# Kernel tuning notes

Measured on AMD Instinct MI355X. Metric: run time of the kernel, lower is better.

The kernel has to match this reference:

```python
import jax, jax.numpy as jnp
import numpy as np

B, S, IN, OUT, H, M = 16, 512, 512, 512, 8, 4
HF = OUT // H  # head_feats = 64


def setup_inputs() -> dict:
    key = jax.random.key(0)
    ks = jax.random.split(key, 12)
    std = 0.02
    queries = jax.random.normal(ks[0], (B, S, IN), jnp.float32)
    keys = jax.random.normal(ks[1], (B, S, IN), jnp.float32)
    timespans = jax.random.uniform(ks[2], (B, S), jnp.float32)
    # causal mask tiled over heads*batch, matching [H*B, S, S] score shape
    attention_masks = jnp.broadcast_to(jnp.tril(jnp.ones((S, S), jnp.float32)), (H * B, S, S))
    event_marks = jax.random.uniform(ks[3], (H * B, 1, S, M), jnp.float32)
    Wq = std * jax.random.normal(ks[4], (IN, OUT), jnp.float32)
    Wk = std * jax.random.normal(ks[5], (IN, OUT), jnp.float32)
    Wv = std * jax.random.normal(ks[6], (IN, OUT), jnp.float32)
    Wt = std * jax.random.normal(ks[7], (IN, OUT), jnp.float32)
    Wi = std * jax.random.normal(ks[8], (HF + 1, M * HF), jnp.float32)  # fc_i weight
    bi = jnp.zeros((M * HF,), jnp.float32)                               # fc_i bias
    weight_i = std * jax.random.normal(ks[9], (M, HF), jnp.float32)
    scale_i = jnp.zeros((M,), jnp.float32)
    return {"queries": queries, "keys": keys, "timespans": timespans,
            "attention_masks": attention_masks, "event_marks": event_marks,
            "Wq": Wq, "Wk": Wk, "Wv": Wv, "Wt": Wt, "Wi": Wi, "bi": bi,
            "weight_i": weight_i, "scale_i": scale_i}


def reference(queries, keys, timespans, attention_masks, event_marks,
              Wq, Wk, Wv, Wt, Wi, bi, weight_i, scale_i):
    # torch's cat(chunk(X, H, dim=2), dim=0) == [B,S,H,HF] -> [H,B,S,HF] -> flat h*B+b
    def split_heads(X):
        return X.reshape(B, S, H, HF).transpose(2, 0, 1, 3)  # [H,B,S,HF]

    Q = split_heads(queries @ Wq)
    K = split_heads(keys @ Wk)
    V = split_heads(keys @ Wv)
    T = split_heads(keys @ Wt)

    scores = jnp.einsum('hbqf,hbkf->hbqk', Q, K) / jnp.sqrt(jnp.float32(OUT))
    mask = attention_masks.reshape(H, B, S, S)
    scores = jnp.where(mask == 0.0, jnp.float32(-2 ** 32 + 1), scores)
    attn = jax.nn.softmax(scores, axis=-1)  # [H,B,Sq,Sk]

    E = jnp.einsum('hbqk,hbkf->hbqf', attn, T)  # events fed to intensity net

    # --- Hawkes intensities ---
    ts = jnp.broadcast_to(timespans[None, :, :, None], (H, B, S, 1))
    mu = jax.nn.sigmoid(jnp.concatenate([E, ts], axis=-1) @ Wi + bi)  # [H,B,S,M*HF]
    mu = mu.reshape(H, B, S, M, HF)  # chunk over marks along feature dim
    scale = jnp.exp(scale_i)  # [M]
    lam = jnp.einsum('hbsmf,mf->hbsm', mu, weight_i) / scale
    lam = scale * jnp.log1p(jnp.exp(lam))  # scaled softplus, [H,B,S,M]

    # mark_inty[h,b,q,k] = sum_m lam[h,b,q,m] * event_marks[h,b,k,m]
    em = event_marks.reshape(H, B, S, M)
    mark_inty = jnp.einsum('hbqm,hbkm->hbqk', lam, em)

    out = jnp.einsum('hbqk,hbkf->hbqf', attn * mark_inty, V)
    out = out.transpose(1, 2, 0, 3).reshape(B, S, OUT) + queries[..., :OUT]
    all_mark_inty = lam.reshape(H * B, S, M)
    return out, all_mark_inty
```

## Files before the change

### kernel.cpp

```cpp
#include <hip/hip_runtime.h>
#include <math.h>

typedef __attribute__((ext_vector_type(8))) short short8;
typedef __attribute__((ext_vector_type(4))) float f32x4;

static __device__ __forceinline__ unsigned short f2bf(float f) {
  unsigned int u = __float_as_uint(f);
  u += 0x7FFFu + ((u >> 16) & 1u);
  return (unsigned short)(u >> 16);
}

static __device__ __forceinline__ void cp16(void* lds, const void* g) {
  __builtin_amdgcn_global_load_lds((const __attribute__((address_space(1))) void*)g,
                                   (__attribute__((address_space(3))) void*)lds,
                                   16, 0, 0);
}

__global__ __launch_bounds__(256) void convert_k(
    const float* __restrict__ Wq, const float* __restrict__ Wk,
    const float* __restrict__ Wv, const float* __restrict__ Wt,
    const float* __restrict__ Wi,
    unsigned short* __restrict__ Wb, unsigned short* __restrict__ WiF)
{
  __shared__ unsigned short tr[64 * 68];
  const int blk = blockIdx.x, tid = threadIdx.x;
  if (blk < 256) {
    int which = blk >> 6, tile = blk & 63;
    int r0 = (tile >> 3) << 6, c0 = (tile & 7) << 6;
    const float* W = (which == 0) ? Wq : (which == 1) ? Wk : (which == 2) ? Wv : Wt;
    const int rr = tid >> 4, cc = (tid & 15) << 2;
#pragma unroll
    for (int u = 0; u < 4; ++u) {
      int r = rr + u * 16;
      float4 v = *(const float4*)(W + (size_t)(r0 + r) * 512 + c0 + cc);
      tr[(cc + 0) * 68 + r] = f2bf(v.x);
      tr[(cc + 1) * 68 + r] = f2bf(v.y);
      tr[(cc + 2) * 68 + r] = f2bf(v.z);
      tr[(cc + 3) * 68 + r] = f2bf(v.w);
    }
    __syncthreads();
    unsigned short* dst = Wb + which * 262144;
#pragma unroll
    for (int u = 0; u < 4; ++u) {
      int c = rr + u * 16;
      ushort4 o = *(const ushort4*)&tr[c * 68 + cc];
      *(ushort4*)(dst + (size_t)(c0 + c) * 512 + r0 + cc) = o;
    }
  } else {
    int e = (blk - 256) * 256 + tid;
    int j = e & 7, ll = (e >> 3) & 63, r = e >> 9;
    int kk = r % 3, nt = r / 3;
    int col = nt * 16 + (ll & 15);
    int k = kk * 32 + (ll >> 4) * 8 + j;
    float val = (k < 64) ? Wi[k * 256 + col] : ((k == 64) ? Wi[16384 + col] : 0.0f);
    WiF[e] = f2bf(val);
  }
}

__global__ __launch_bounds__(256) void proj_mfma(
    const float* __restrict__ qin, const float* __restrict__ kin,
    const unsigned short* __restrict__ Wb,
    unsigned short* __restrict__ Qg, unsigned short* __restrict__ Kg,
    unsigned short* __restrict__ Vt, unsigned short* __restrict__ Tt)
{
  const int which = blockIdx.z;
  const float* A = (which == 0) ? qin : kin;
  const unsigned short* W = Wb + which * 262144;
  const int row0 = blockIdx.x * 128;
  const int col0 = blockIdx.y * 128;
  const int tid = threadIdx.x;
  const int wv = tid >> 6, l = tid & 63;
  const int quad = l >> 4, lc = l & 15;
  const int wm = wv >> 1, wn = wv & 1;

  __shared__ unsigned short Asm[2][128 * 32];
  __shared__ unsigned short Bsm[2][128 * 32];

  const int e2 = tid + 256;
  const int br0 = tid >> 2, bg0 = (tid & 3) ^ (br0 & 3);
  const int br1 = e2 >> 2,  bg1 = (e2 & 3) ^ (br1 & 3);
  f32x4 acc[4][4] = {};

  cp16(&Bsm[0][tid * 8], W + (size_t)(col0 + br0) * 512 + bg0 * 8);
  cp16(&Bsm[0][e2 * 8], W + (size_t)(col0 + br1) * 512 + bg1 * 8);
#pragma unroll
  for (int u = 0; u < 4; ++u) {
    int i = tid + u * 256, r = i >> 3, c4 = i & 7;
    float4 v = *(const float4*)(A + (size_t)(row0 + r) * 512 + c4 * 4);
    ushort4 o;
    o.x = f2bf(v.x); o.y = f2bf(v.y); o.z = f2bf(v.z); o.w = f2bf(v.w);
    *(ushort4*)&Asm[0][r * 32 + (((c4 >> 1) ^ (r & 3)) << 3) + ((c4 & 1) << 2)] = o;
  }
  __syncthreads();

  const int xk = lc & 3;
  for (int ks = 0; ks < 16; ++ks) {
    const int cur = ks & 1, nxt = cur ^ 1;
    float4 av[4];
    if (ks < 15) {
      const int k1 = (ks + 1) << 5;
      cp16(&Bsm[nxt][tid * 8], W + (size_t)(col0 + br0) * 512 + k1 + bg0 * 8);
      cp16(&Bsm[nxt][e2 * 8], W + (size_t)(col0 + br1) * 512 + k1 + bg1 * 8);
#pragma unroll
      for (int u = 0; u < 4; ++u) {
        int i = tid + u * 256, r = i >> 3, c4 = i & 7;
        av[u] = *(const float4*)(A + (size_t)(row0 + r) * 512 + k1 + c4 * 4);
      }
    }
    short8 a[4], b[4];
#pragma unroll
    for (int mi = 0; mi < 4; ++mi)
      a[mi] = *(const short8*)&Asm[cur][(wm * 64 + mi * 16 + lc) * 32 + ((quad ^ xk) << 3)];
#pragma unroll
    for (int nj = 0; nj < 4; ++nj)
      b[nj] = *(const short8*)&Bsm[cur][(wn * 64 + nj * 16 + lc) * 32 + ((quad ^ xk) << 3)];
#pragma unroll
    for (int mi = 0; mi < 4; ++mi)
#pragma unroll
      for (int nj = 0; nj < 4; ++nj)
        acc[mi][nj] = __builtin_amdgcn_mfma_f32_16x16x32_bf16(a[mi], b[nj], acc[mi][nj], 0, 0, 0);
    if (ks < 15) {
#pragma unroll
      for (int u = 0; u < 4; ++u) {
        int i = tid + u * 256, r = i >> 3, c4 = i & 7;
        ushort4 o;
        o.x = f2bf(av[u].x); o.y = f2bf(av[u].y); o.z = f2bf(av[u].z); o.w = f2bf(av[u].w);
        *(ushort4*)&Asm[nxt][r * 32 + (((c4 >> 1) ^ (r & 3)) << 3) + ((c4 & 1) << 2)] = o;
      }
    }
    __syncthreads();
  }

  const int h = (col0 >> 6) + wn;
  const int bidx = row0 >> 9;
  const int hb = h * 16 + bidx;
  if (which < 2) {
    unsigned short* C = (which == 0) ? Qg : Kg;
    const float os = (which == 0) ? 0.044194173824159216f : 1.0f;
#pragma unroll
    for (int mi = 0; mi < 4; ++mi) {
      int sbase = (row0 & 511) + wm * 64 + mi * 16 + quad * 4;
#pragma unroll
      for (int nj = 0; nj < 4; ++nj) {
        size_t base = (size_t)hb * 32768 + (size_t)sbase * 64 + nj * 16 + lc;
#pragma unroll
        for (int reg = 0; reg < 4; ++reg)
          C[base + (size_t)reg * 64] = f2bf(acc[mi][nj][reg] * os);
      }
    }
  } else {
    unsigned short* C = (which == 2) ? Vt : Tt;
    unsigned short* scr = wn ? Bsm[0] : Asm[0];
    const int sb = (row0 & 511) + wm * 64;
    __syncthreads();
#pragma unroll
    for (int round = 0; round < 2; ++round) {
      if (wm == round) {
#pragma unroll
        for (int mi = 0; mi < 4; ++mi)
#pragma unroll
          for (int nj = 0; nj < 4; ++nj)
#pragma unroll
            for (int reg = 0; reg < 4; ++reg) {
              int f = nj * 16 + lc, s = mi * 16 + quad * 4 + reg;
              int g = (s >> 3) ^ (f & 7);
              scr[f * 64 + g * 8 + (s & 7)] = f2bf(acc[mi][nj][reg]);
            }
#pragma unroll
        for (int it = 0; it < 8; ++it) {
          int fl = it * 8 + (l >> 3);
          int gg = (l & 7) ^ (fl & 7);
          short8 v = *(const short8*)&scr[fl * 64 + gg * 8];
          *(short8*)(C + (size_t)hb * 32768 + (size_t)fl * 512 + sb + (l & 7) * 8) = v;
        }
      }
      __syncthreads();
    }
  }
}

__global__ __launch_bounds__(256, 2) void attn_fused(
    const unsigned short* __restrict__ Qg, const unsigned short* __restrict__ Kg,
    const unsigned short* __restrict__ Vtg, const unsigned short* __restrict__ Ttg,
    const unsigned short* __restrict__ WiF,
    const float* __restrict__ bi, const float* __restrict__ wim,
    const float* __restrict__ sci, const float* __restrict__ tsp,
    const float* __restrict__ em, const float* __restrict__ queries,
    float* __restrict__ out, float* __restrict__ lamout)
{
  const int hb = blockIdx.x;
  const int y = blockIdx.y;
  const int qb = (y == 0) ? 3 : (y == 1) ? 2 : (y == 2) ? 0 : 1;
  const int q0 = qb << 7;
  const int kts = 2 * qb + 2;
  const int tid = threadIdx.x, wv = tid >> 6, l = tid & 63;
  const int quad = l >> 4, lc = l & 15;
  const int xg = lc & 7;

  __shared__ unsigned short Qs[8192];
  __shared__ unsigned short Ks[2][4096];
  __shared__ unsigned short TVs[2][4096];
  __shared__ unsigned short Wl[4][3072];
  __shared__ float emS[2][256];

  const int e1 = tid + 256;
  const int sr0 = tid >> 3, sg0 = (tid & 7) ^ (sr0 & 7);
  const int sr1 = e1 >> 3,  sg1 = (e1 & 7) ^ (sr1 & 7);
  const int sqk0 = sr0 * 64 + sg0 * 8,  sqk1 = sr1 * 64 + sg1 * 8;
  const int stv0 = sr0 * 512 + sg0 * 8, stv1 = sr1 * 512 + sg1 * 8;

  const unsigned short* KgB = Kg + (size_t)hb * 32768;
  const unsigned short* TgB = Ttg + (size_t)hb * 32768;
  const unsigned short* VgB = Vtg + (size_t)hb * 32768;

  const unsigned short* Qbase = Qg + (size_t)hb * 32768 + q0 * 64;
#pragma unroll
  for (int u = 0; u < 4; ++u) {
    int e = tid + u * 256;
    int r = e >> 3, g = (e & 7) ^ (r & 7);
    cp16(&Qs[e * 8], Qbase + r * 64 + g * 8);
  }
  cp16(&Ks[0][tid * 8], KgB + sqk0);
  cp16(&Ks[0][e1 * 8], KgB + sqk1);
  cp16(&TVs[0][tid * 8], TgB + stv0);
  cp16(&TVs[0][e1 * 8], TgB + stv1);
  __syncthreads();

  short8 aq[2][2];
#pragma unroll
  for (int rt = 0; rt < 2; ++rt)
#pragma unroll
    for (int kk = 0; kk < 2; ++kk)
      aq[rt][kk] = *(const short8*)&Qs[(wv * 32 + rt * 16 + lc) * 64 + ((kk * 4 + quad) ^ xg) * 8];

  f32x4 Eacc[2][4] = {};
  float lsum[2][4] = {};

  for (int kt = 0; kt < kts; ++kt) {
    const int cur = kt & 1, nxt = cur ^ 1;
    const int k0 = kt << 6;
    if (kt + 1 < kts) {
      const int k1 = (kt + 1) << 6;
      cp16(&Ks[nxt][tid * 8], KgB + k1 * 64 + sqk0);
      cp16(&Ks[nxt][e1 * 8], KgB + k1 * 64 + sqk1);
      cp16(&TVs[nxt][tid * 8], TgB + k1 + stv0);
      cp16(&TVs[nxt][e1 * 8], TgB + k1 + stv1);
    }
    f32x4 sc[2][4] = {};
#pragma unroll
    for (int kk = 0; kk < 2; ++kk)
#pragma unroll
      for (int nj = 0; nj < 4; ++nj) {
        short8 b = *(const short8*)&Ks[cur][(nj * 16 + lc) * 64 + ((kk * 4 + quad) ^ xg) * 8];
        sc[0][nj] = __builtin_amdgcn_mfma_f32_16x16x32_bf16(aq[0][kk], b, sc[0][nj], 0, 0, 0);
        sc[1][nj] = __builtin_amdgcn_mfma_f32_16x16x32_bf16(aq[1][kk], b, sc[1][nj], 0, 0, 0);
      }
#pragma unroll
    for (int rt = 0; rt < 2; ++rt) {
      const int gq = q0 + wv * 32 + rt * 16 + quad * 4;
#pragma unroll
      for (int nj = 0; nj < 4; ++nj) {
        int col = nj * 16 + lc;
#pragma unroll
        for (int reg = 0; reg < 4; ++reg) {
          float pv = __expf(sc[rt][nj][reg]);
          if (k0 + col > gq + reg) pv = 0.0f;
          lsum[rt][reg] += pv;
          int row = rt * 16 + quad * 4 + reg;
          int gp = (nj * 2 + (lc >> 3)) ^ (row & 7);
          Wl[wv][row * 96 + gp * 8 + (lc & 7)] = f2bf(pv);
        }
      }
    }
#pragma unroll
    for (int rt = 0; rt < 2; ++rt)
#pragma unroll
      for (int kk = 0; kk < 2; ++kk) {
        short8 a = *(const short8*)&Wl[wv][(rt * 16 + lc) * 96 + ((kk * 4 + quad) ^ xg) * 8];
#pragma unroll
        for (int fj = 0; fj < 4; ++fj) {
          short8 b = *(const short8*)&TVs[cur][(fj * 16 + lc) * 64 + ((kk * 4 + quad) ^ xg) * 8];
          Eacc[rt][fj] = __builtin_amdgcn_mfma_f32_16x16x32_bf16(a, b, Eacc[rt][fj], 0, 0, 0);
        }
      }
    __syncthreads();
  }

  float inv[2][4];
#pragma unroll
  for (int rt = 0; rt < 2; ++rt)
#pragma unroll
    for (int reg = 0; reg < 4; ++reg) {
      float s = lsum[rt][reg];
#pragma unroll
      for (int off = 1; off < 16; off <<= 1) s += __shfl_xor(s, off);
      inv[rt][reg] = 1.0f / s;
    }

#pragma unroll
  for (int rt = 0; rt < 2; ++rt)
#pragma unroll
    for (int reg = 0; reg < 4; ++reg) {
      int row = rt * 16 + quad * 4 + reg;
      int gq = q0 + wv * 32 + rt * 16 + quad * 4;
      unsigned short* rp = &Wl[wv][row * 96];
#pragma unroll
      for (int fj = 0; fj < 4; ++fj) {
        int gp = (fj * 2 + (lc >> 3)) ^ (row & 7);
        rp[gp * 8 + (lc & 7)] = f2bf(Eacc[rt][fj][reg] * inv[rt][reg]);
      }
      float tsv = (lc == 0) ? tsp[(hb & 15) * 512 + gq + reg] : 0.0f;
      int gt = 8 + ((lc >> 3) ^ (row & 3));
      rp[gt * 8 + (lc & 7)] = f2bf(tsv);
      int gz = 8 + ((2 + (lc >> 3)) ^ (row & 3));
      rp[gz * 8 + (lc & 7)] = 0;
    }

  float lam4[2][4][4];
#pragma unroll
  for (int rt = 0; rt < 2; ++rt) {
    short8 ia[3];
    ia[0] = *(const short8*)&Wl[wv][(rt * 16 + lc) * 96 + ((0 + quad) ^ xg) * 8];
    ia[1] = *(const short8*)&Wl[wv][(rt * 16 + lc) * 96 + ((4 + quad) ^ xg) * 8];
    ia[2] = *(const short8*)&Wl[wv][(rt * 16 + lc) * 96 + (8 + (quad ^ (lc & 3))) * 8];
    float lac[4][4] = {};
#pragma unroll
    for (int nt = 0; nt < 16; ++nt) {
      f32x4 iacc = {};
#pragma unroll
      for (int kk = 0; kk < 3; ++kk) {
        short8 b = *(const short8*)(WiF + ((nt * 3 + kk) * 64 + l) * 8);
        iacc = __builtin_amdgcn_mfma_f32_16x16x32_bf16(ia[kk], b, iacc, 0, 0, 0);
      }
      float bvv = bi[nt * 16 + lc];
      float wmv = wim[nt * 16 + lc];
#pragma unroll
      for (int reg = 0; reg < 4; ++reg) {
        float mu = 1.0f / (1.0f + __expf(-(iacc[reg] + bvv)));
        lac[reg][nt >> 2] += mu * wmv;
      }
    }
#pragma unroll
    for (int m = 0; m < 4; ++m) {
      float scv = __expf(sci[m]);
#pragma unroll
      for (int reg = 0; reg < 4; ++reg) {
        float s = lac[reg][m];
#pragma unroll
        for (int off = 1; off < 16; off <<= 1) s += __shfl_xor(s, off);
        float z = s / scv;
        float sp = (z > 20.0f) ? z : log1pf(__expf(z));
        lam4[rt][reg][m] = scv * sp;
      }
    }
    if (lc < 4) {
      int gq = q0 + wv * 32 + rt * 16 + quad * 4;
#pragma unroll
      for (int reg = 0; reg < 4; ++reg) {
        float v = (lc == 0) ? lam4[rt][reg][0] : (lc == 1) ? lam4[rt][reg][1]
                : (lc == 2) ? lam4[rt][reg][2] : lam4[rt][reg][3];
        lamout[((size_t)hb * 512 + gq + reg) * 4 + lc] = v;
      }
    }
#pragma unroll
    for (int reg = 0; reg < 4; ++reg)
#pragma unroll
      for (int m = 0; m < 4; ++m)
        lam4[rt][reg][m] *= inv[rt][reg];
  }

  cp16(&Ks[0][tid * 8], KgB + sqk0);
  cp16(&Ks[0][e1 * 8], KgB + sqk1);
  cp16(&TVs[0][tid * 8], VgB + stv0);
  cp16(&TVs[0][e1 * 8], VgB + stv1);
  emS[0][tid] = em[(size_t)hb * 2048 + tid];
  __syncthreads();

  f32x4 Oacc[2][4] = {};
  for (int kt = 0; kt < kts; ++kt) {
    const int cur = kt & 1, nxt = cur ^ 1;
    const int k0 = kt << 6;
    if (kt + 1 < kts) {
      const int k1 = (kt + 1) << 6;
      cp16(&Ks[nxt][tid * 8], KgB + k1 * 64 + sqk0);
      cp16(&Ks[nxt][e1 * 8], KgB + k1 * 64 + sqk1);
      cp16(&TVs[nxt][tid * 8], VgB + k1 + stv0);
      cp16(&TVs[nxt][e1 * 8], VgB + k1 + stv1);
      emS[nxt][tid] = em[(size_t)hb * 2048 + k1 * 4 + tid];
    }
    f32x4 sc[2][4] = {};
#pragma unroll
    for (int kk = 0; kk < 2; ++kk)
#pragma unroll
      for (int nj = 0; nj < 4; ++nj) {
        short8 b = *(const short8*)&Ks[cur][(nj * 16 + lc) * 64 + ((kk * 4 + quad) ^ xg) * 8];
        sc[0][nj] = __builtin_amdgcn_mfma_f32_16x16x32_bf16(aq[0][kk], b, sc[0][nj], 0, 0, 0);
        sc[1][nj] = __builtin_amdgcn_mfma_f32_16x16x32_bf16(aq[1][kk], b, sc[1][nj], 0, 0, 0);
      }
#pragma unroll
    for (int rt = 0; rt < 2; ++rt) {
      const int gq = q0 + wv * 32 + rt * 16 + quad * 4;
#pragma unroll
      for (int nj = 0; nj < 4; ++nj) {
        int col = nj * 16 + lc;
        float4 emv = *(const float4*)&emS[cur][col * 4];
#pragma unroll
        for (int reg = 0; reg < 4; ++reg) {
          float pv = __expf(sc[rt][nj][reg]);
          if (k0 + col > gq + reg) pv = 0.0f;
          float mk = lam4[rt][reg][0] * emv.x + lam4[rt][reg][1] * emv.y +
                     lam4[rt][reg][2] * emv.z + lam4[rt][reg][3] * emv.w;
          int row = rt * 16 + quad * 4 + reg;
          int gp = (nj * 2 + (lc >> 3)) ^ (row & 7);
          Wl[wv][row * 96 + gp * 8 + (lc & 7)] = f2bf(pv * mk);
        }
      }
    }
#pragma unroll
    for (int rt = 0; rt < 2; ++rt)
#pragma unroll
      for (int kk = 0; kk < 2; ++kk) {
        short8 a = *(const short8*)&Wl[wv][(rt * 16 + lc) * 96 + ((kk * 4 + quad) ^ xg) * 8];
#pragma unroll
        for (int fj = 0; fj < 4; ++fj) {
          short8 b = *(const short8*)&TVs[cur][(fj * 16 + lc) * 64 + ((kk * 4 + quad) ^ xg) * 8];
          Oacc[rt][fj] = __builtin_amdgcn_mfma_f32_16x16x32_bf16(a, b, Oacc[rt][fj], 0, 0, 0);
        }
      }
    __syncthreads();
  }

  const int h = hb >> 4, bidx = hb & 15;
#pragma unroll
  for (int rt = 0; rt < 2; ++rt) {
    const int gq = q0 + wv * 32 + rt * 16 + quad * 4;
#pragma unroll
    for (int reg = 0; reg < 4; ++reg) {
      size_t o = (size_t)bidx * 262144 + (size_t)(gq + reg) * 512 + h * 64 + lc;
#pragma unroll
      for (int fj = 0; fj < 4; ++fj)
        out[o + fj * 16] = Oacc[rt][fj][reg] + queries[o + fj * 16];
    }
  }
}

extern "C" void kernel_launch(void* const* d_in, const int* in_sizes, int n_in,
                              void* d_out, int out_size, void* d_ws, size_t ws_size,
                              hipStream_t stream)
{
  (void)in_sizes; (void)n_in; (void)out_size; (void)ws_size;
  const float* queries = (const float*)d_in[0];
  const float* keys    = (const float*)d_in[1];
  const float* tsp     = (const float*)d_in[2];
  const float* em      = (const float*)d_in[4];
  const float* Wq      = (const float*)d_in[5];
  const float* Wk      = (const float*)d_in[6];
  const float* Wv      = (const float*)d_in[7];
  const float* Wt      = (const float*)d_in[8];
  const float* Wi      = (const float*)d_in[9];
  const float* bi      = (const float*)d_in[10];
  const float* wim     = (const float*)d_in[11];
  const float* sci     = (const float*)d_in[12];
  float* out = (float*)d_out;

  char* w = (char*)d_ws;
  unsigned short* Qg  = (unsigned short*)(w + 0);
  unsigned short* Kg  = (unsigned short*)(w + 8388608);
  unsigned short* Vt  = (unsigned short*)(w + 16777216);
  unsigned short* Tt  = (unsigned short*)(w + 25165824);
  unsigned short* Wb  = (unsigned short*)(w + 33554432);
  unsigned short* WiF = (unsigned short*)(w + 35651584);

  convert_k<<<352, 256, 0, stream>>>(Wq, Wk, Wv, Wt, Wi, Wb, WiF);
  proj_mfma<<<dim3(64, 4, 4), 256, 0, stream>>>(queries, keys, Wb, Qg, Kg, Vt, Tt);
  attn_fused<<<dim3(128, 4), 256, 0, stream>>>(Qg, Kg, Vt, Tt, WiF, bi, wim, sci,
                                               tsp, em, queries, out,
                                               out + 4194304);
}
```

Before: 303.4 us.

## Skip fully masked causal tiles per wave, fold log2e into weights, add setprio

```diff
diff --git a/kernel.cpp b/kernel.cpp
--- a/kernel.cpp
+++ b/kernel.cpp
@@ -3,11 +3,24 @@
 
 typedef __attribute__((ext_vector_type(8))) short short8;
 typedef __attribute__((ext_vector_type(4))) float f32x4;
+
+#define L2E 1.4426950408889634f
 
 static __device__ __forceinline__ unsigned short f2bf(float f) {
   unsigned int u = __float_as_uint(f);
   u += 0x7FFFu + ((u >> 16) & 1u);
   return (unsigned short)(u >> 16);
+}
+
+static __device__ __forceinline__ float fast_exp2(float x) {
+#if __has_builtin(__builtin_amdgcn_exp2f)
+  return __builtin_amdgcn_exp2f(x);
+#else
+  return exp2f(x);
+#endif
+}
+static __device__ __forceinline__ float fast_rcp(float x) {
+  return __builtin_amdgcn_rcpf(x);
 }
 
 static __device__ __forceinline__ void cp16(void* lds, const void* g) {
@@ -53,7 +66,7 @@
     int col = nt * 16 + (ll & 15);
     int k = kk * 32 + (ll >> 4) * 8 + j;
     float val = (k < 64) ? Wi[k * 256 + col] : ((k == 64) ? Wi[16384 + col] : 0.0f);
-    WiF[e] = f2bf(val);
+    WiF[e] = f2bf(val * L2E);
   }
 }
 
@@ -114,11 +127,13 @@
 #pragma unroll
     for (int nj = 0; nj < 4; ++nj)
       b[nj] = *(const short8*)&Bsm[cur][(wn * 64 + nj * 16 + lc) * 32 + ((quad ^ xk) << 3)];
+    __builtin_amdgcn_s_setprio(1);
 #pragma unroll
     for (int mi = 0; mi < 4; ++mi)
 #pragma unroll
       for (int nj = 0; nj < 4; ++nj)
         acc[mi][nj] = __builtin_amdgcn_mfma_f32_16x16x32_bf16(a[mi], b[nj], acc[mi][nj], 0, 0, 0);
+    __builtin_amdgcn_s_setprio(0);
     if (ks < 15) {
 #pragma unroll
       for (int u = 0; u < 4; ++u) {
@@ -136,7 +151,7 @@
   const int hb = h * 16 + bidx;
   if (which < 2) {
     unsigned short* C = (which == 0) ? Qg : Kg;
-    const float os = (which == 0) ? 0.044194173824159216f : 1.0f;
+    const float os = (which == 0) ? 0.044194173824159216f * L2E : 1.0f;
 #pragma unroll
     for (int mi = 0; mi < 4; ++mi) {
       int sbase = (row0 & 511) + wm * 64 + mi * 16 + quad * 4;
@@ -196,8 +211,8 @@
   const int tid = threadIdx.x, wv = tid >> 6, l = tid & 63;
   const int quad = l >> 4, lc = l & 15;
   const int xg = lc & 7;
-
-  __shared__ unsigned short Qs[8192];
+  const int wrow0 = q0 + wv * 32;
+
   __shared__ unsigned short Ks[2][4096];
   __shared__ unsigned short TVs[2][4096];
   __shared__ unsigned short Wl[4][3072];
@@ -213,25 +228,21 @@
   const unsigned short* TgB = Ttg + (size_t)hb * 32768;
   const unsigned short* VgB = Vtg + (size_t)hb * 32768;
 
-  const unsigned short* Qbase = Qg + (size_t)hb * 32768 + q0 * 64;
-#pragma unroll
-  for (int u = 0; u < 4; ++u) {
-    int e = tid + u * 256;
-    int r = e >> 3, g = (e & 7) ^ (r & 7);
-    cp16(&Qs[e * 8], Qbase + r * 64 + g * 8);
-  }
   cp16(&Ks[0][tid * 8], KgB + sqk0);
   cp16(&Ks[0][e1 * 8], KgB + sqk1);
   cp16(&TVs[0][tid * 8], TgB + stv0);
   cp16(&TVs[0][e1 * 8], TgB + stv1);
+
+  short8 aq[2][2];
+  {
+    const unsigned short* Qp = Qg + (size_t)hb * 32768;
+#pragma unroll
+    for (int rt = 0; rt < 2; ++rt)
+#pragma unroll
+      for (int kk = 0; kk < 2; ++kk)
+        aq[rt][kk] = *(const short8*)(Qp + (size_t)(wrow0 + rt * 16 + lc) * 64 + (kk * 4 + quad) * 8);
+  }
   __syncthreads();
-
-  short8 aq[2][2];
-#pragma unroll
-  for (int rt = 0; rt < 2; ++rt)
-#pragma unroll
-    for (int kk = 0; kk < 2; ++kk)
-      aq[rt][kk] = *(const short8*)&Qs[(wv * 32 + rt * 16 + lc) * 64 + ((kk * 4 + quad) ^ xg) * 8];
 
   f32x4 Eacc[2][4] = {};
   float lsum[2][4] = {};
@@ -246,43 +257,62 @@
       cp16(&TVs[nxt][tid * 8], TgB + k1 + stv0);
       cp16(&TVs[nxt][e1 * 8], TgB + k1 + stv1);
     }
-    f32x4 sc[2][4] = {};
-#pragma unroll
-    for (int kk = 0; kk < 2; ++kk)
-#pragma unroll
-      for (int nj = 0; nj < 4; ++nj) {
-        short8 b = *(const short8*)&Ks[cur][(nj * 16 + lc) * 64 + ((kk * 4 + quad) ^ xg) * 8];
-        sc[0][nj] = __builtin_amdgcn_mfma_f32_16x16x32_bf16(aq[0][kk], b, sc[0][nj], 0, 0, 0);
-        sc[1][nj] = __builtin_amdgcn_mfma_f32_16x16x32_bf16(aq[1][kk], b, sc[1][nj], 0, 0, 0);
-      }
-#pragma unroll
-    for (int rt = 0; rt < 2; ++rt) {
-      const int gq = q0 + wv * 32 + rt * 16 + quad * 4;
-#pragma unroll
-      for (int nj = 0; nj < 4; ++nj) {
-        int col = nj * 16 + lc;
-#pragma unroll
-        for (int reg = 0; reg < 4; ++reg) {
-          float pv = __expf(sc[rt][nj][reg]);
-          if (k0 + col > gq + reg) pv = 0.0f;
-          lsum[rt][reg] += pv;
-          int row = rt * 16 + quad * 4 + reg;
-          int gp = (nj * 2 + (lc >> 3)) ^ (row & 7);
-          Wl[wv][row * 96 + gp * 8 + (lc & 7)] = f2bf(pv);
-        }
-      }
-    }
-#pragma unroll
-    for (int rt = 0; rt < 2; ++rt)
-#pragma unroll
-      for (int kk = 0; kk < 2; ++kk) {
-        short8 a = *(const short8*)&Wl[wv][(rt * 16 + lc) * 96 + ((kk * 4 + quad) ^ xg) * 8];
-#pragma unroll
-        for (int fj = 0; fj < 4; ++fj) {
-          short8 b = *(const short8*)&TVs[cur][(fj * 16 + lc) * 64 + ((kk * 4 + quad) ^ xg) * 8];
-          Eacc[rt][fj] = __builtin_amdgcn_mfma_f32_16x16x32_bf16(a, b, Eacc[rt][fj], 0, 0, 0);
-        }
-      }
+    if (k0 <= wrow0 + 31) {
+      f32x4 sc[2][4] = {};
+      __builtin_amdgcn_s_setprio(1);
+#pragma unroll
+      for (int kk = 0; kk < 2; ++kk)
+#pragma unroll
+        for (int nj = 0; nj < 4; ++nj) {
+          const bool l0 = (k0 + nj * 16) <= (wrow0 + 15);
+          const bool l1 = (k0 + nj * 16) <= (wrow0 + 31);
+          if (l1) {
+            short8 b = *(const short8*)&Ks[cur][(nj * 16 + lc) * 64 + ((kk * 4 + quad) ^ xg) * 8];
+            if (l0) sc[0][nj] = __builtin_amdgcn_mfma_f32_16x16x32_bf16(aq[0][kk], b, sc[0][nj], 0, 0, 0);
+            sc[1][nj] = __builtin_amdgcn_mfma_f32_16x16x32_bf16(aq[1][kk], b, sc[1][nj], 0, 0, 0);
+          }
+        }
+      __builtin_amdgcn_s_setprio(0);
+#pragma unroll
+      for (int rt = 0; rt < 2; ++rt) {
+        const int gq = wrow0 + rt * 16 + quad * 4;
+#pragma unroll
+        for (int nj = 0; nj < 4; ++nj) {
+          const int col = nj * 16 + lc;
+          if ((k0 + nj * 16) <= (wrow0 + rt * 16 + 15)) {
+#pragma unroll
+            for (int reg = 0; reg < 4; ++reg) {
+              float pv = fast_exp2(sc[rt][nj][reg]);
+              if (k0 + col > gq + reg) pv = 0.0f;
+              lsum[rt][reg] += pv;
+              int row = rt * 16 + quad * 4 + reg;
+              int gp = (nj * 2 + (lc >> 3)) ^ (row & 7);
+              Wl[wv][row * 96 + gp * 8 + (lc & 7)] = f2bf(pv);
+            }
+          } else {
+#pragma unroll
+            for (int reg = 0; reg < 4; ++reg) {
+              int row = rt * 16 + quad * 4 + reg;
+              int gp = (nj * 2 + (lc >> 3)) ^ (row & 7);
+              Wl[wv][row * 96 + gp * 8 + (lc & 7)] = 0;
+            }
+          }
+        }
+      }
+      __builtin_amdgcn_s_setprio(1);
+#pragma unroll
+      for (int rt = 0; rt < 2; ++rt)
+#pragma unroll
+        for (int kk = 0; kk < 2; ++kk) {
+          short8 a = *(const short8*)&Wl[wv][(rt * 16 + lc) * 96 + ((kk * 4 + quad) ^ xg) * 8];
+#pragma unroll
+          for (int fj = 0; fj < 4; ++fj) {
+            short8 b = *(const short8*)&TVs[cur][(fj * 16 + lc) * 64 + ((kk * 4 + quad) ^ xg) * 8];
+            Eacc[rt][fj] = __builtin_amdgcn_mfma_f32_16x16x32_bf16(a, b, Eacc[rt][fj], 0, 0, 0);
+          }
+        }
+      __builtin_amdgcn_s_setprio(0);
+    }
     __syncthreads();
   }
 
@@ -294,7 +324,7 @@
       float s = lsum[rt][reg];
 #pragma unroll
       for (int off = 1; off < 16; off <<= 1) s += __shfl_xor(s, off);
-      inv[rt][reg] = 1.0f / s;
+      inv[rt][reg] = fast_rcp(s);
     }
 
 #pragma unroll
@@ -327,28 +357,31 @@
 #pragma unroll
     for (int nt = 0; nt < 16; ++nt) {
       f32x4 iacc = {};
+      __builtin_amdgcn_s_setprio(1);
 #pragma unroll
       for (int kk = 0; kk < 3; ++kk) {
         short8 b = *(const short8*)(WiF + ((nt * 3 + kk) * 64 + l) * 8);
         iacc = __builtin_amdgcn_mfma_f32_16x16x32_bf16(ia[kk], b, iacc, 0, 0, 0);
       }
-      float bvv = bi[nt * 16 + lc];
+      __builtin_amdgcn_s_setprio(0);
+      float bvv = bi[nt * 16 + lc] * L2E;
       float wmv = wim[nt * 16 + lc];
 #pragma unroll
       for (int reg = 0; reg < 4; ++reg) {
-        float mu = 1.0f / (1.0f + __expf(-(iacc[reg] + bvv)));
+        float mu = fast_rcp(1.0f + fast_exp2(-(iacc[reg] + bvv)));
         lac[reg][nt >> 2] += mu * wmv;
       }
     }
 #pragma unroll
     for (int m = 0; m < 4; ++m) {
       float scv = __expf(sci[m]);
+      float rscv = fast_rcp(scv);
 #pragma unroll
       for (int reg = 0; reg < 4; ++reg) {
         float s = lac[reg][m];
 #pragma unroll
         for (int off = 1; off < 16; off <<= 1) s += __shfl_xor(s, off);
-        float z = s / scv;
+        float z = s * rscv;
         float sp = (z > 20.0f) ? z : log1pf(__expf(z));
         lam4[rt][reg][m] = scv * sp;
       }
@@ -388,45 +421,66 @@
       cp16(&TVs[nxt][e1 * 8], VgB + k1 + stv1);
       emS[nxt][tid] = em[(size_t)hb * 2048 + k1 * 4 + tid];
     }
-    f32x4 sc[2][4] = {};
-#pragma unroll
-    for (int kk = 0; kk < 2; ++kk)
+    if (k0 <= wrow0 + 31) {
+      f32x4 sc[2][4] = {};
+      __builtin_amdgcn_s_setprio(1);
+#pragma unroll
+      for (int kk = 0; kk < 2; ++kk)
+#pragma unroll
+        for (int nj = 0; nj < 4; ++nj) {
+          const bool l0 = (k0 + nj * 16) <= (wrow0 + 15);
+          const bool l1 = (k0 + nj * 16) <= (wrow0 + 31);
+          if (l1) {
+            short8 b = *(const short8*)&Ks[cur][(nj * 16 + lc) * 64 + ((kk * 4 + quad) ^ xg) * 8];
+            if (l0) sc[0][nj] = __builtin_amdgcn_mfma_f32_16x16x32_bf16(aq[0][kk], b, sc[0][nj], 0, 0, 0);
+            sc[1][nj] = __builtin_amdgcn_mfma_f32_16x16x32_bf16(aq[1][kk], b, sc[1][nj], 0, 0, 0);
+          }
+        }
+      __builtin_amdgcn_s_setprio(0);
 #pragma unroll
       for (int nj = 0; nj < 4; ++nj) {
-        short8 b = *(const short8*)&Ks[cur][(nj * 16 + lc) * 64 + ((kk * 4 + quad) ^ xg) * 8];
-        sc[0][nj] = __builtin_amdgcn_mfma_f32_16x16x32_bf16(aq[0][kk], b, sc[0][nj], 0, 0, 0);
-        sc[1][nj] = __builtin_amdgcn_mfma_f32_16x16x32_bf16(aq[1][kk], b, sc[1][nj], 0, 0, 0);
-      }
-#pragma unroll
-    for (int rt = 0; rt < 2; ++rt) {
-      const int gq = q0 + wv * 32 + rt * 16 + quad * 4;
-#pragma unroll
-      for (int nj = 0; nj < 4; ++nj) {
-        int col = nj * 16 + lc;
-        float4 emv = *(const float4*)&emS[cur][col * 4];
-#pragma unroll
-        for (int reg = 0; reg < 4; ++reg) {
-          float pv = __expf(sc[rt][nj][reg]);
-          if (k0 + col > gq + reg) pv = 0.0f;
-          float mk = lam4[rt][reg][0] * emv.x + lam4[rt][reg][1] * emv.y +
-                     lam4[rt][reg][2] * emv.z + lam4[rt][reg][3] * emv.w;
-          int row = rt * 16 + quad * 4 + reg;
-          int gp = (nj * 2 + (lc >> 3)) ^ (row & 7);
-          Wl[wv][row * 96 + gp * 8 + (lc & 7)] = f2bf(pv * mk);
-        }
-      }
-    }
-#pragma unroll
-    for (int rt = 0; rt < 2; ++rt)
-#pragma unroll
-      for (int kk = 0; kk < 2; ++kk) {
-        short8 a = *(const short8*)&Wl[wv][(rt * 16 + lc) * 96 + ((kk * 4 + quad) ^ xg) * 8];
-#pragma unroll
-        for (int fj = 0; fj < 4; ++fj) {
-          short8 b = *(const short8*)&TVs[cur][(fj * 16 + lc) * 64 + ((kk * 4 + quad) ^ xg) * 8];
-          Oacc[rt][fj] = __builtin_amdgcn_mfma_f32_16x16x32_bf16(a, b, Oacc[rt][fj], 0, 0, 0);
-        }
-      }
+        const int col = nj * 16 + lc;
+        const bool l1 = (k0 + nj * 16) <= (wrow0 + 31);
+        float4 emv;
+        if (l1) emv = *(const float4*)&emS[cur][col * 4];
+#pragma unroll
+        for (int rt = 0; rt < 2; ++rt) {
+          const int gq = wrow0 + rt * 16 + quad * 4;
+          if ((k0 + nj * 16) <= (wrow0 + rt * 16 + 15)) {
+#pragma unroll
+            for (int reg = 0; reg < 4; ++reg) {
+              float pv = fast_exp2(sc[rt][nj][reg]);
+              if (k0 + col > gq + reg) pv = 0.0f;
+              float mk = lam4[rt][reg][0] * emv.x + lam4[rt][reg][1] * emv.y +
+                         lam4[rt][reg][2] * emv.z + lam4[rt][reg][3] * emv.w;
+              int row = rt * 16 + quad * 4 + reg;
+              int gp = (nj * 2 + (lc >> 3)) ^ (row & 7);
+              Wl[wv][row * 96 + gp * 8 + (lc & 7)] = f2bf(pv * mk);
+            }
+          } else {
+#pragma unroll
+            for (int reg = 0; reg < 4; ++reg) {
+              int row = rt * 16 + quad * 4 + reg;
+              int gp = (nj * 2 + (lc >> 3)) ^ (row & 7);
+              Wl[wv][row * 96 + gp * 8 + (lc & 7)] = 0;
+            }
+          }
+        }
+      }
+      __builtin_amdgcn_s_setprio(1);
+#pragma unroll
+      for (int rt = 0; rt < 2; ++rt)
+#pragma unroll
+        for (int kk = 0; kk < 2; ++kk) {
+          short8 a = *(const short8*)&Wl[wv][(rt * 16 + lc) * 96 + ((kk * 4 + quad) ^ xg) * 8];
+#pragma unroll
+          for (int fj = 0; fj < 4; ++fj) {
+            short8 b = *(const short8*)&TVs[cur][(fj * 16 + lc) * 64 + ((kk * 4 + quad) ^ xg) * 8];
+            Oacc[rt][fj] = __builtin_amdgcn_mfma_f32_16x16x32_bf16(a, b, Oacc[rt][fj], 0, 0, 0);
+          }
+        }
+      __builtin_amdgcn_s_setprio(0);
+    }
     __syncthreads();
   }
 
```

Result: no change. 305.1 us (+0.6%).
